# Kernel tuning notes

Hardware: AMD Instinct MI355X
Metric: run time of the kernel (lower is better)

## Reference

```python
import jax, jax.numpy as jnp
import numpy as np

B, S, K, N = 4, 2048, 4096, 4096


def setup_inputs() -> dict:
    key = jax.random.key(0)
    kx, kw = jax.random.split(key)
    # int8 activations and weights in [-127, 127), matching torch.randint(-127,127,...)
    x = jax.random.randint(kx, (B, S, K), -127, 127, dtype=jnp.int32).astype(jnp.int8)
    weight = jax.random.randint(kw, (N, K), -127, 127, dtype=jnp.int32).astype(jnp.int8)
    bias = jnp.zeros((1, N), dtype=jnp.int32)
    out_scale = jnp.ones((), dtype=jnp.float32)
    bias_scale = jnp.ones((), dtype=jnp.float32)
    return {"x": x, "weight": weight, "bias": bias,
            "out_scale": out_scale, "bias_scale": bias_scale}


def reference(x, weight, bias, out_scale, bias_scale):
    # Flatten leading dims: [B, S, K] -> [M, K]
    x_shape = x.shape
    x2 = x.reshape(-1, x_shape[-1])
    acc = jax.lax.dot_general(
        x2, weight,
        dimension_numbers=(((1,), (1,)), ((), ())),
        preferred_element_type=jnp.int32,
    )  # [M, N] int32
    # Fused epilogue: y = round(out_scale * acc + bias_scale * bias) -> int32
    y = jnp.round(acc.astype(jnp.float32) * out_scale
                  + bias.astype(jnp.float32) * bias_scale).astype(jnp.int32)
    return y.reshape(*x_shape[:-1], -1)
```

## Files before the change

### kernel.cpp

```cpp
#include <hip/hip_runtime.h>
#include <stdint.h>


typedef int v4i __attribute__((ext_vector_type(4)));

#define BM 256
#define BN 256
#define BK 128
#define KK 4096
#define KT (KK / BK)

__global__ __launch_bounds__(256)
void pack_i32_to_i8(const v4i* __restrict__ src, int* __restrict__ dst, int n4) {
    int i = blockIdx.x * blockDim.x + threadIdx.x;
    if (i >= n4) return;
    v4i a = src[i];
    dst[i] = (a[0] & 0xff) | ((a[1] & 0xff) << 8) | ((a[2] & 0xff) << 16) | (a[3] << 24);
}

__device__ __forceinline__ void gld_lds16(const void* g, void* lds) {
    __builtin_amdgcn_global_load_lds(
        (const __attribute__((address_space(1))) unsigned int*)g,
        (__attribute__((address_space(3))) unsigned int*)lds,
        16, 0, 0);
}

#define MFMA_I8 __builtin_amdgcn_mfma_i32_16x16x64_i8
#define BARRIER() __builtin_amdgcn_s_barrier()
#define LGKM0() asm volatile("s_waitcnt lgkmcnt(0)" ::: "memory")
#define PRIO(x) __builtin_amdgcn_s_setprio(x)

__global__ __launch_bounds__(512, 2)
void w8a8_gemm_kernel(const int8_t* __restrict__ X,
                      const int8_t* __restrict__ W,
                      const int*    __restrict__ bias,
                      const float*  __restrict__ out_scale_p,
                      const float*  __restrict__ bias_scale_p,
                      int*          __restrict__ Y,
                      int M, int N)
{
    __shared__ __align__(16) int8_t sA[2 * BM * BK];
    __shared__ __align__(16) int8_t sB[2 * BN * BK];

    const int tid = threadIdx.x;

    const int nbx = N / BN;
    const int nby = M / BM;
    int bx, by;
    {
        const int wg = blockIdx.x;
        if (nbx == 16 && nby == 32) {
            const int x = wg & 7;
            const int k = wg >> 3;
            bx = ((x & 1) << 3) | (k & 7);
            by = ((x >> 1) << 3) | (k >> 3);
        } else { bx = wg % nbx; by = wg / nbx; }
    }
    const int bn = bx * BN;
    const int bm = by * BM;

    const float out_scale  = *out_scale_p;
    const float bias_scale = *bias_scale_p;

    const int8_t* Abase = X + (size_t)bm * KK;
    const int8_t* Bbase = W + (size_t)bn * KK;

    const int r0  = tid >> 3;
    const int j0  = tid & 7;
    const int sw  = (j0 ^ (r0 & 7)) << 4;
    const size_t gOff = (size_t)r0 * KK + sw;
    const int  lOff = tid << 4;

#define STAGE(gbase, lds, t, h) do {                                              \
        const int8_t* _g = (gbase) + (size_t)((h) * 128) * KK                     \
                                   + (size_t)(t) * BK + gOff;                     \
        int8_t* _l = (lds) + (((t) & 1) << 15) + ((h) << 14) + lOff;              \
        gld_lds16(_g,                  _l);                                       \
        gld_lds16(_g + (size_t)64 * KK, _l + 8192);                               \
    } while (0)

    const int w    = tid >> 6;
    const int l    = tid & 63;
    const int wmw  = w >> 2;
    const int wnw  = w & 3;
    const int tm   = l & 15;
    const int quad = l >> 4;
    const int s3   = tm & 7;
    const int xo0  = ( quad      ^ s3) << 4;
    const int xo1  = ((quad + 4) ^ s3) << 4;
    const int rowA = ((wmw << 7) + tm) << 7;
    const int rowB = ((wnw << 6) + tm) << 7;

    v4i acc[8][4];
    const v4i vz = {0, 0, 0, 0};
#pragma unroll
    for (int i = 0; i < 8; ++i)
#pragma unroll
        for (int j = 0; j < 4; ++j)
            acc[i][j] = vz;

    STAGE(Abase, sA, 0, 0); STAGE(Abase, sA, 0, 1);
    STAGE(Bbase, sB, 0, 0); STAGE(Bbase, sB, 0, 1);
    STAGE(Bbase, sB, 1, 0); STAGE(Bbase, sB, 1, 1);
    asm volatile("s_waitcnt vmcnt(4)" ::: "memory");
    BARRIER();

#pragma unroll 2
    for (int t = 0; t < KT; ++t) {
        const int bo = (t & 1) << 15;
        const int8_t* sAb = sA + bo;
        const int8_t* sBb = sB + bo;
        v4i a0[4], a1[4], b0[4], b1[4];

#pragma unroll
        for (int i = 0; i < 4; ++i)
            a0[i] = *(const v4i*)(sAb + rowA + i * 2048 + xo0);
#pragma unroll
        for (int j = 0; j < 4; ++j)
            b0[j] = *(const v4i*)(sBb + rowB + j * 2048 + xo0);
        if (t + 1 < KT) STAGE(Abase, sA, t + 1, 0);
        BARRIER();
        LGKM0();
        PRIO(1);
#pragma unroll
        for (int i = 0; i < 4; ++i)
#pragma unroll
            for (int j = 0; j < 4; ++j)
                acc[i][j] = MFMA_I8(a0[i], b0[j], acc[i][j], 0, 0, 0);
        PRIO(0);
        BARRIER();

#pragma unroll
        for (int i = 0; i < 4; ++i)
            a1[i] = *(const v4i*)(sAb + rowA + (i + 4) * 2048 + xo0);
#pragma unroll
        for (int j = 0; j < 4; ++j)
            b1[j] = *(const v4i*)(sBb + rowB + j * 2048 + xo1);
        if (t + 1 < KT) STAGE(Abase, sA, t + 1, 1);
        BARRIER();
        LGKM0();
        PRIO(1);
#pragma unroll
        for (int i = 0; i < 4; ++i)
#pragma unroll
            for (int j = 0; j < 4; ++j)
                acc[i + 4][j] = MFMA_I8(a1[i], b0[j], acc[i + 4][j], 0, 0, 0);
        PRIO(0);
        BARRIER();

#pragma unroll
        for (int i = 0; i < 4; ++i)
            a0[i] = *(const v4i*)(sAb + rowA + i * 2048 + xo1);
        if (t + 2 < KT) STAGE(Bbase, sB, t + 2, 0);
        BARRIER();
        LGKM0();
        PRIO(1);
#pragma unroll
        for (int i = 0; i < 4; ++i)
#pragma unroll
            for (int j = 0; j < 4; ++j)
                acc[i][j] = MFMA_I8(a0[i], b1[j], acc[i][j], 0, 0, 0);
        PRIO(0);
        BARRIER();

#pragma unroll
        for (int i = 0; i < 4; ++i)
            a1[i] = *(const v4i*)(sAb + rowA + (i + 4) * 2048 + xo1);
        if (t + 2 < KT) {
            STAGE(Bbase, sB, t + 2, 1);
            asm volatile("s_waitcnt vmcnt(4)" ::: "memory");
        } else {
            asm volatile("s_waitcnt vmcnt(0)" ::: "memory");
        }
        BARRIER();
        LGKM0();
        PRIO(1);
#pragma unroll
        for (int i = 0; i < 4; ++i)
#pragma unroll
            for (int j = 0; j < 4; ++j)
                acc[i + 4][j] = MFMA_I8(a1[i], b1[j], acc[i + 4][j], 0, 0, 0);
        PRIO(0);
        BARRIER();
    }
#undef STAGE

    float bb[4];
#pragma unroll
    for (int j = 0; j < 4; ++j)
        bb[j] = (float)bias[bn + (wnw << 6) + (j << 4) + tm] * bias_scale;
#pragma unroll
    for (int i = 0; i < 8; ++i) {
        const int mb = bm + (wmw << 7) + (i << 4) + (quad << 2);
#pragma unroll
        for (int r = 0; r < 4; ++r) {
            int* yrow = Y + (size_t)(mb + r) * N + bn + (wnw << 6) + tm;
#pragma unroll
            for (int j = 0; j < 4; ++j) {
                const float v = (float)acc[i][j][r] * out_scale + bb[j];
                yrow[j << 4] = (int)rintf(v);
            }
        }
    }
}

extern "C" void kernel_launch(void* const* d_in, const int* in_sizes, int n_in,
                              void* d_out, int out_size, void* d_ws, size_t ws_size,
                              hipStream_t stream) {
    const int* x32 = (const int*)d_in[0];
    const int* w32 = (const int*)d_in[1];
    const int*    bias = (const int*)d_in[2];
    const float*  os   = (const float*)d_in[3];
    const float*  bs   = (const float*)d_in[4];
    int* out = (int*)d_out;

    const int K = KK;
    const int M = in_sizes[0] / K;
    const int N = in_sizes[1] / K;
    const int nx = in_sizes[0];
    const int nw = in_sizes[1];

    int8_t* x8 = (int8_t*)d_ws;
    int8_t* w8 = x8 + (size_t)nx;

    pack_i32_to_i8<<<dim3(nx / 4 / 256), dim3(256), 0, stream>>>((const v4i*)x32, (int*)x8, nx / 4);
    pack_i32_to_i8<<<dim3(nw / 4 / 256), dim3(256), 0, stream>>>((const v4i*)w32, (int*)w8, nw / 4);

    dim3 grid((N / BN) * (M / BM));
    dim3 block(512);
    hipLaunchKernelGGL(w8a8_gemm_kernel, grid, block, 0, stream,
                       x8, w8, bias, os, bs, out, M, N);
}
```

Measured before the change: 385.3 us.

## Replace staggered ping-pong K-loop with a simple single-barrier double buffer

The fine-grained K-loop is removed. It had four barrier-separated MFMA phases, s_setprio, B tiles prefetched two steps ahead and explicit vmcnt waits. In its place, each iteration issues all A and B global-to-LDS loads for the next tile, runs two larger 8x4 MFMA blocks over the current tile, and ends with one __syncthreads. This cuts barrier count and schedule complexity, but the loads now only overlap with one tile of compute. It also relies on __syncthreads to drain the async LDS loads, and it loses the wave-priority interleaving.

```diff
diff --git a/kernel.cpp b/kernel.cpp
--- a/kernel.cpp
+++ b/kernel.cpp
@@ -26,9 +26,6 @@
 }
 
 #define MFMA_I8 __builtin_amdgcn_mfma_i32_16x16x64_i8
-#define BARRIER() __builtin_amdgcn_s_barrier()
-#define LGKM0() asm volatile("s_waitcnt lgkmcnt(0)" ::: "memory")
-#define PRIO(x) __builtin_amdgcn_s_setprio(x)
 
 __global__ __launch_bounds__(512, 2)
 void w8a8_gemm_kernel(const int8_t* __restrict__ X,
@@ -101,87 +98,45 @@
 
     STAGE(Abase, sA, 0, 0); STAGE(Abase, sA, 0, 1);
     STAGE(Bbase, sB, 0, 0); STAGE(Bbase, sB, 0, 1);
-    STAGE(Bbase, sB, 1, 0); STAGE(Bbase, sB, 1, 1);
-    asm volatile("s_waitcnt vmcnt(4)" ::: "memory");
-    BARRIER();
+    __syncthreads();
 
 #pragma unroll 2
     for (int t = 0; t < KT; ++t) {
         const int bo = (t & 1) << 15;
         const int8_t* sAb = sA + bo;
         const int8_t* sBb = sB + bo;
-        v4i a0[4], a1[4], b0[4], b1[4];
 
+        if (t + 1 < KT) {
+            STAGE(Abase, sA, t + 1, 0); STAGE(Abase, sA, t + 1, 1);
+            STAGE(Bbase, sB, t + 1, 0); STAGE(Bbase, sB, t + 1, 1);
+        }
+        __builtin_amdgcn_sched_barrier(0);
+
+        v4i a[8], b[4];
 #pragma unroll
-        for (int i = 0; i < 4; ++i)
-            a0[i] = *(const v4i*)(sAb + rowA + i * 2048 + xo0);
+        for (int i = 0; i < 8; ++i)
+            a[i] = *(const v4i*)(sAb + rowA + i * 2048 + xo0);
 #pragma unroll
         for (int j = 0; j < 4; ++j)
-            b0[j] = *(const v4i*)(sBb + rowB + j * 2048 + xo0);
-        if (t + 1 < KT) STAGE(Abase, sA, t + 1, 0);
-        BARRIER();
-        LGKM0();
-        PRIO(1);
+            b[j] = *(const v4i*)(sBb + rowB + j * 2048 + xo0);
 #pragma unroll
-        for (int i = 0; i < 4; ++i)
+        for (int i = 0; i < 8; ++i)
 #pragma unroll
             for (int j = 0; j < 4; ++j)
-                acc[i][j] = MFMA_I8(a0[i], b0[j], acc[i][j], 0, 0, 0);
-        PRIO(0);
-        BARRIER();
-
+                acc[i][j] = MFMA_I8(a[i], b[j], acc[i][j], 0, 0, 0);
 #pragma unroll
-        for (int i = 0; i < 4; ++i)
-            a1[i] = *(const v4i*)(sAb + rowA + (i + 4) * 2048 + xo0);
+        for (int i = 0; i < 8; ++i)
+            a[i] = *(const v4i*)(sAb + rowA + i * 2048 + xo1);
 #pragma unroll
         for (int j = 0; j < 4; ++j)
-            b1[j] = *(const v4i*)(sBb + rowB + j * 2048 + xo1);
-        if (t + 1 < KT) STAGE(Abase, sA, t + 1, 1);
-        BARRIER();
-        LGKM0();
-        PRIO(1);
+            b[j] = *(const v4i*)(sBb + rowB + j * 2048 + xo1);
 #pragma unroll
-        for (int i = 0; i < 4; ++i)
+        for (int i = 0; i < 8; ++i)
 #pragma unroll
             for (int j = 0; j < 4; ++j)
-                acc[i + 4][j] = MFMA_I8(a1[i], b0[j], acc[i + 4][j], 0, 0, 0);
-        PRIO(0);
-        BARRIER();
+                acc[i][j] = MFMA_I8(a[i], b[j], acc[i][j], 0, 0, 0);
 
-#pragma unroll
-        for (int i = 0; i < 4; ++i)
-            a0[i] = *(const v4i*)(sAb + rowA + i * 2048 + xo1);
-        if (t + 2 < KT) STAGE(Bbase, sB, t + 2, 0);
-        BARRIER();
-        LGKM0();
-        PRIO(1);
-#pragma unroll
-        for (int i = 0; i < 4; ++i)
-#pragma unroll
-            for (int j = 0; j < 4; ++j)
-                acc[i][j] = MFMA_I8(a0[i], b1[j], acc[i][j], 0, 0, 0);
-        PRIO(0);
-        BARRIER();
-
-#pragma unroll
-        for (int i = 0; i < 4; ++i)
-            a1[i] = *(const v4i*)(sAb + rowA + (i + 4) * 2048 + xo1);
-        if (t + 2 < KT) {
-            STAGE(Bbase, sB, t + 2, 1);
-            asm volatile("s_waitcnt vmcnt(4)" ::: "memory");
-        } else {
-            asm volatile("s_waitcnt vmcnt(0)" ::: "memory");
-        }
-        BARRIER();
-        LGKM0();
-        PRIO(1);
-#pragma unroll
-        for (int i = 0; i < 4; ++i)
-#pragma unroll
-            for (int j = 0; j < 4; ++j)
-                acc[i + 4][j] = MFMA_I8(a1[i], b1[j], acc[i + 4][j], 0, 0, 0);
-        PRIO(0);
-        BARRIER();
+        __syncthreads();
     }
 #undef STAGE
 
```

Result: slower. 396.3 us (+2.8%).
